# Kernel tuning notes

Measured on AMD Instinct MI355X. Metric: run time of the kernel, lower is better.

Reference implementation:

```python
import jax, jax.numpy as jnp
import numpy as np

B, N1, N2, E = 8, 32, 32, 256
H = 8                 # num_heads == args.vir_heads
KD = E // H           # key dim per head = 32
HD = E // H           # head dim (value_dim == embed_dim)
L = N1 * N2           # 1024 tokens
SCALING = KD ** -0.5
LN_EPS = 1e-5


def _rel_pos_2d():
    # RetNetRelPosDeform2D with zero offsets (vir_use_deformable=False)
    half = 1.0 / 10000.0 ** jnp.linspace(0.0, 1.0, KD // 2)
    angle = jnp.repeat(half, 2)                                   # (KD,) interleaved pairs
    decay = jnp.log(1.0 - 2.0 ** (-2.0 - 5.0 * jnp.arange(H, dtype=jnp.float32) / H))  # (H,)
    i1 = jnp.arange(N1, dtype=jnp.float32)
    i2 = jnp.arange(N2, dtype=jnp.float32)
    index_k = (i1[:, None] + i2[None, :]).reshape(L)              # (L,)
    sin_k = jnp.sin(index_k[:, None] * angle[None, :])            # (L, KD)
    cos_k = jnp.cos(index_k[:, None] * angle[None, :])
    # zero offsets => index_q == index_k, broadcast over (B, H)
    sin_q = sin_k[None, None]                                     # (1,1,L,KD)
    cos_q = cos_k[None, None]
    # Manhattan distance decay mask on the 2D grid
    d = (jnp.abs(i1[:, None, None, None] - i1[None, None, :, None])
         + jnp.abs(i2[None, :, None, None] - i2[None, None, None, :])).reshape(L, L)
    mask = jnp.exp(d[None, :, :] * decay[:, None, None])          # (H, L, L)
    mask = jnp.nan_to_num(mask)
    mask = mask / jnp.sqrt(mask.sum(-1, keepdims=True))
    return sin_q, cos_q, sin_k, cos_k, mask


def rotate_every_two(x):
    x1 = x[..., ::2]
    x2 = x[..., 1::2]
    return jnp.stack((-x2, x1), axis=-1).reshape(x.shape)


def theta_shift(x, sin, cos):
    return x * cos + rotate_every_two(x) * sin


def setup_inputs() -> dict:
    key = jax.random.key(0)
    ks = jax.random.split(key, 5)
    gain_qkv = 2.0 ** -2.5 * (6.0 / (E + E)) ** 0.5  # xavier_uniform bound scale
    gain_o = 2.0 ** -1 * (6.0 / (E + E)) ** 0.5
    x = jax.random.normal(ks[0], (B, N1, N2, E), dtype=jnp.float32)
    Wq = jax.random.uniform(ks[1], (E, E), jnp.float32, -gain_qkv, gain_qkv)
    Wk = jax.random.uniform(ks[2], (E, E), jnp.float32, -gain_qkv, gain_qkv)
    Wv = jax.random.uniform(ks[3], (E, E), jnp.float32, -gain_qkv, gain_qkv)
    Wo = jax.random.uniform(ks[4], (E, E), jnp.float32, -gain_o, gain_o)
    ln_g = jnp.ones((HD,), jnp.float32)
    ln_b = jnp.zeros((HD,), jnp.float32)
    return {"x": x, "Wq": Wq, "Wk": Wk, "Wv": Wv, "Wo": Wo, "ln_g": ln_g, "ln_b": ln_b}


def reference(x, Wq, Wk, Wv, Wo, ln_g, ln_b):
    sin_q, cos_q, sin_k, cos_k, mask = _rel_pos_2d()
    xf = x.reshape(B, L, E)
    q = (xf @ Wq.T).reshape(B, L, H, KD).transpose(0, 2, 1, 3)    # (B,H,L,KD)
    k = (xf @ Wk.T * SCALING).reshape(B, L, H, KD).transpose(0, 2, 1, 3)
    vr = (xf @ Wv.T).reshape(B, L, H, HD).transpose(0, 2, 1, 3)   # (B,H,L,HD)
    qr = theta_shift(q, sin_q, cos_q)
    kr = theta_shift(k, sin_k[None, None], cos_k[None, None])
    qk = jnp.einsum('bhqd,bhkd->bhqk', qr, kr) * mask[None]       # (B,H,L,L)
    den = jnp.clip(jax.lax.stop_gradient(jnp.abs(qk)).sum(-1, keepdims=True), 1.0, 5e4)
    qk = qk / den
    out = jnp.einsum('bhqk,bhkd->bhqd', qk, vr).transpose(0, 2, 1, 3)  # (B,L,H,HD)
    mu = out.mean(-1, keepdims=True)
    var = out.var(-1, keepdims=True)
    out = (out - mu) / jnp.sqrt(var + LN_EPS) * ln_g + ln_b       # per-head LayerNorm
    out = jax.nn.gelu(out.reshape(B, L, H * HD), approximate=False)
    out = out @ Wo.T
    return out.reshape(B, N1, N2, E)
```

## Files before the change

### kernel.cpp

```cpp
#include <hip/hip_runtime.h>
#include <math.h>

typedef unsigned short u16;
typedef unsigned int u32;
typedef __bf16 bf16x8 __attribute__((ext_vector_type(8)));
typedef float f32x4 __attribute__((ext_vector_type(4)));

#define LOG2E 1.44269504088896f
#define SCALING 0.17677669529663687f
#define LOG2_10000 13.287712379549449f

__device__ __forceinline__ float bf2f(u16 v) {
    u32 u = ((u32)v) << 16; float f; __builtin_memcpy(&f, &u, 4); return f;
}
__device__ __forceinline__ u16 f2bf(float f) {
    u32 u; __builtin_memcpy(&u, &f, 4);
    u = u + 0x7FFFu + ((u >> 16) & 1u);
    return (u16)(u >> 16);
}
__device__ __forceinline__ f32x4 mfma16(bf16x8 a, bf16x8 b, f32x4 c) {
    return __builtin_amdgcn_mfma_f32_16x16x32_bf16(a, b, c, 0, 0, 0);
}
__device__ __forceinline__ float decay_l2(int h) {
    return logf(1.0f - exp2f(-2.0f - 0.625f * (float)h)) * LOG2E;
}

__global__ __launch_bounds__(256) void mask_rsq_kernel(float* __restrict__ rsq) {
    int gw = (blockIdx.x * 256 + threadIdx.x) >> 6;
    int lane = threadIdx.x & 63;
    int h = gw >> 10, q = gw & 1023;
    float dec = decay_l2(h);
    int q1 = q >> 5, q2 = q & 31;
    float s = 0.0f;
    for (int k = lane; k < 1024; k += 64) {
        int k1 = k >> 5, k2 = k & 31;
        float d = (float)(abs(q1 - k1) + abs(q2 - k2));
        s += exp2f(dec * d);
    }
#pragma unroll
    for (int m = 32; m; m >>= 1) s += __shfl_xor(s, m);
    if (lane == 0) rsq[gw] = rsqrtf(s);
}

__global__ __launch_bounds__(256) void mask_build_kernel(const float* __restrict__ rsq,
                                                         u16* __restrict__ mask) {
    int t = blockIdx.x * 256 + threadIdx.x;
    int row = t >> 7;
    int k0 = (t & 127) << 3;
    int h = row >> 10, q = row & 1023;
    float dec = decay_l2(h);
    float r = rsq[row];
    int q1 = q >> 5, q2 = q & 31;
    int k1 = k0 >> 5, k2b = k0 & 31;
    union { int4 v; u16 s[8]; } tmp;
#pragma unroll
    for (int i = 0; i < 8; i++) {
        float d = (float)(abs(q1 - k1) + abs(q2 - (k2b + i)));
        tmp.s[i] = f2bf(exp2f(dec * d) * r);
    }
    *(int4*)&mask[(long)row * 1024 + k0] = tmp.v;
}

template<int AF32>
__global__ __launch_bounds__(256) void gemm_bt_kernel(
    const void* __restrict__ Av,
    const float* __restrict__ W0, const float* __restrict__ W1, const float* __restrict__ W2,
    u16* __restrict__ O0, u16* __restrict__ O1, u16* __restrict__ O2,
    float* __restrict__ Of, int mode_base) {
    __shared__ u16 As[64 * 136];
    __shared__ u16 Ws[64 * 136];
    int z = blockIdx.z;
    const float* W = (z == 0) ? W0 : (z == 1) ? W1 : W2;
    u16* O = (z == 0) ? O0 : (z == 1) ? O1 : O2;
    int mode = mode_base + z;
    int r0 = blockIdx.x * 64, n0 = blockIdx.y * 64;
    int tid = threadIdx.x;
    int w = tid >> 6, lane = tid & 63, ln = lane & 15, quad = lane >> 4;
    f32x4 acc[4] = {};
#pragma unroll
    for (int ch = 0; ch < 2; ch++) {
        int k0 = ch * 128;
        if (ch) __syncthreads();
#pragma unroll
        for (int i = 0; i < 8; i++) {
            int c = tid + i * 256;
            int row = c >> 5, seg = c & 31;
            float4 wv = *(const float4*)&W[(long)(n0 + row) * 256 + k0 + seg * 4];
            union { int2 v; u16 s[4]; } t;
            t.s[0] = f2bf(wv.x); t.s[1] = f2bf(wv.y); t.s[2] = f2bf(wv.z); t.s[3] = f2bf(wv.w);
            *(int2*)&Ws[row * 136 + seg * 4] = t.v;
        }
        if (AF32) {
            const float* A = (const float*)Av;
#pragma unroll
            for (int i = 0; i < 8; i++) {
                int c = tid + i * 256;
                int row = c >> 5, seg = c & 31;
                float4 av = *(const float4*)&A[(long)(r0 + row) * 256 + k0 + seg * 4];
                union { int2 v; u16 s[4]; } t;
                t.s[0] = f2bf(av.x); t.s[1] = f2bf(av.y); t.s[2] = f2bf(av.z); t.s[3] = f2bf(av.w);
                *(int2*)&As[row * 136 + seg * 4] = t.v;
            }
        } else {
            const u16* A = (const u16*)Av;
#pragma unroll
            for (int i = 0; i < 4; i++) {
                int c = tid + i * 256;
                int row = c >> 4, seg = c & 15;
                *(int4*)&As[row * 136 + seg * 8] = *(const int4*)&A[(long)(r0 + row) * 256 + k0 + seg * 8];
            }
        }
        __syncthreads();
#pragma unroll
        for (int kt = 0; kt < 4; kt++) {
            bf16x8 a = *(const bf16x8*)&As[(w * 16 + ln) * 136 + kt * 32 + quad * 8];
#pragma unroll
            for (int nt = 0; nt < 4; nt++) {
                bf16x8 b = *(const bf16x8*)&Ws[(nt * 16 + ln) * 136 + kt * 32 + quad * 8];
                acc[nt] = mfma16(a, b, acc[nt]);
            }
        }
    }
    int rowg = r0 + w * 16 + quad * 4;
    if (mode == 3) {
#pragma unroll
        for (int nt = 0; nt < 4; nt++) {
            int e = n0 + nt * 16 + ln;
#pragma unroll
            for (int r = 0; r < 4; r++)
                Of[(long)(rowg + r) * 256 + e] = acc[nt][r];
        }
        return;
    }
    float scl = (mode == 1) ? SCALING : 1.0f;
#pragma unroll
    for (int nt = 0; nt < 4; nt++) {
        int e = n0 + nt * 16 + ln;
        int d = e & 31, hh = e >> 5;
        float ang = exp2f(-LOG2_10000 * (1.0f / 15.0f) * (float)(d >> 1));
#pragma unroll
        for (int r = 0; r < 4; r++) {
            int gi = rowg + r;
            int b = gi >> 10, l = gi & 1023;
            float v = acc[nt][r] * scl;
            float p = __shfl_xor(v, 1);
            float res;
            if (mode == 2) {
                res = v;
            } else {
                float idx = (float)((l >> 5) + (l & 31));
                float sv, cv;
                __sincosf(idx * ang, &sv, &cv);
                res = (d & 1) ? (v * cv + p * sv) : (v * cv - p * sv);
            }
            O[(((long)(b * 8 + hh)) * 1024 + l) * 32 + d] = f2bf(res);
        }
    }
}

__global__ __launch_bounds__(256) void attn_kernel(
    const u16* __restrict__ qr, const u16* __restrict__ kr, const u16* __restrict__ vr,
    const u16* __restrict__ mask, const float* __restrict__ lng, const float* __restrict__ lnb,
    u16* __restrict__ out) {
    __shared__ u16 Qs[64 * 40];
    __shared__ u16 Ks[64 * 40];
    __shared__ u16 Vt[32 * 72];
    __shared__ u16 Ps[64 * 72];
    int b = blockIdx.z, h = blockIdx.y, q0 = blockIdx.x * 64;
    int tid = threadIdx.x, w = tid >> 6, lane = tid & 63, ln = lane & 15, quad = lane >> 4;
    long bh = b * 8 + h;
    const u16* qb = qr + bh * 32768;
    const u16* kb = kr + bh * 32768;
    const u16* vb = vr + bh * 32768;
    const u16* mb = mask + (long)h * 1048576;
    {
        int row = tid >> 2, seg = tid & 3;
        *(int4*)&Qs[row * 40 + seg * 8] = *(const int4*)&qb[(q0 + row) * 32 + seg * 8];
    }
    __syncthreads();
    int m0 = w * 16;
    bf16x8 aq = *(const bf16x8*)&Qs[(m0 + ln) * 40 + quad * 8];
    f32x4 accO[2] = {};
    float den[4] = {0.f, 0.f, 0.f, 0.f};
    for (int kt = 0; kt < 16; kt++) {
        int k0 = kt * 64;
        {
            int row = tid >> 2, seg = tid & 3;
            *(int4*)&Ks[row * 40 + seg * 8] = *(const int4*)&kb[(k0 + row) * 32 + seg * 8];
            union { int4 v; u16 s[8]; } vv;
            vv.v = *(const int4*)&vb[(k0 + row) * 32 + seg * 8];
#pragma unroll
            for (int i = 0; i < 8; i++) Vt[(seg * 8 + i) * 72 + row] = vv.s[i];
        }
        __syncthreads();
        f32x4 zero = {};
#pragma unroll
        for (int nt = 0; nt < 4; nt++) {
            bf16x8 bk = *(const bf16x8*)&Ks[(nt * 16 + ln) * 40 + quad * 8];
            f32x4 s = mfma16(aq, bk, zero);
            int col = nt * 16 + ln;
            const u16* mrow = mb + (long)(q0 + m0 + quad * 4) * 1024 + k0 + col;
#pragma unroll
            for (int r = 0; r < 4; r++) {
                float p = s[r] * bf2f(mrow[(long)r * 1024]);
                den[r] += fabsf(p);
                Ps[(m0 + quad * 4 + r) * 72 + col] = f2bf(p);
            }
        }
#pragma unroll
        for (int c2 = 0; c2 < 2; c2++) {
            bf16x8 ap = *(const bf16x8*)&Ps[(m0 + ln) * 72 + c2 * 32 + quad * 8];
#pragma unroll
            for (int nv = 0; nv < 2; nv++) {
                bf16x8 bv = *(const bf16x8*)&Vt[(nv * 16 + ln) * 72 + c2 * 32 + quad * 8];
                accO[nv] = mfma16(ap, bv, accO[nv]);
            }
        }
        __syncthreads();
    }
#pragma unroll
    for (int m = 1; m < 16; m <<= 1)
#pragma unroll
        for (int r = 0; r < 4; r++) den[r] += __shfl_xor(den[r], m);
    float o[2][4], s1[4], s2[4];
#pragma unroll
    for (int r = 0; r < 4; r++) {
        float id = 1.0f / fminf(fmaxf(den[r], 1.0f), 50000.0f);
        o[0][r] = accO[0][r] * id;
        o[1][r] = accO[1][r] * id;
        s1[r] = o[0][r] + o[1][r];
        s2[r] = o[0][r] * o[0][r] + o[1][r] * o[1][r];
    }
#pragma unroll
    for (int m = 1; m < 16; m <<= 1)
#pragma unroll
        for (int r = 0; r < 4; r++) {
            s1[r] += __shfl_xor(s1[r], m);
            s2[r] += __shfl_xor(s2[r], m);
        }
    float g[2] = {lng[ln], lng[16 + ln]};
    float bb[2] = {lnb[ln], lnb[16 + ln]};
#pragma unroll
    for (int r = 0; r < 4; r++) {
        float mean = s1[r] * (1.0f / 32.0f);
        float var = s2[r] * (1.0f / 32.0f) - mean * mean;
        float rstd = rsqrtf(var + 1e-5f);
        int l = q0 + m0 + quad * 4 + r;
#pragma unroll
        for (int nv = 0; nv < 2; nv++) {
            float x = (o[nv][r] - mean) * rstd * g[nv] + bb[nv];
            float ge = 0.5f * x * (1.0f + erff(x * 0.70710678118654752f));
            out[((long)(b * 1024 + l)) * 256 + h * 32 + nv * 16 + ln] = f2bf(ge);
        }
    }
}

extern "C" void kernel_launch(void* const* d_in, const int* in_sizes, int n_in,
                              void* d_out, int out_size, void* d_ws, size_t ws_size,
                              hipStream_t stream) {
    const float* x   = (const float*)d_in[0];
    const float* Wq  = (const float*)d_in[1];
    const float* Wk  = (const float*)d_in[2];
    const float* Wv  = (const float*)d_in[3];
    const float* Wo  = (const float*)d_in[4];
    const float* lng = (const float*)d_in[5];
    const float* lnb = (const float*)d_in[6];
    float* outp = (float*)d_out;

    u16* qr    = (u16*)d_ws;
    u16* kr    = qr + 2097152;
    u16* vr    = kr + 2097152;
    u16* attn  = vr + 2097152;
    u16* maskb = attn + 2097152;
    float* rsq = (float*)(maskb + 8388608);

    mask_rsq_kernel<<<2048, 256, 0, stream>>>(rsq);
    mask_build_kernel<<<4096, 256, 0, stream>>>(rsq, maskb);
    gemm_bt_kernel<1><<<dim3(128, 4, 3), 256, 0, stream>>>(x, Wq, Wk, Wv, qr, kr, vr, nullptr, 0);
    attn_kernel<<<dim3(16, 8, 8), 256, 0, stream>>>(qr, kr, vr, maskb, lng, lnb, attn);
    gemm_bt_kernel<0><<<dim3(128, 4, 1), 256, 0, stream>>>(attn, Wo, Wo, Wo, nullptr, nullptr, nullptr, outp, 3);
}
```

Measured before the change: 137.9 us.

## Compute decay mask on the fly in attention and pre-convert inputs to bf16

Removes the two kernels that built a 16 MB bf16 decay mask and instead computes mask values inside the attention kernel. It uses a per-block exp2 table indexed by Manhattan distance and a separable row-sum normalisation (the sum factors into Ss[q1]*Ss[q2]). Adds a conversion kernel that casts x and all weights to bf16 once, so the GEMMs load bf16 directly. The GEMM grid is reordered so that blocks sharing the same A rows run adjacently. The aim is to cut mask bandwidth and launches, at the cost of extra LDS lookups and integer work in the attention inner loop.

After: 128.9 us. -6.5%, faster.

```diff
diff --git a/kernel.cpp b/kernel.cpp
--- a/kernel.cpp
+++ b/kernel.cpp
@@ -6,13 +6,10 @@
 typedef __bf16 bf16x8 __attribute__((ext_vector_type(8)));
 typedef float f32x4 __attribute__((ext_vector_type(4)));
 
+#define SCALING 0.17677669529663687f
 #define LOG2E 1.44269504088896f
-#define SCALING 0.17677669529663687f
 #define LOG2_10000 13.287712379549449f
 
-__device__ __forceinline__ float bf2f(u16 v) {
-    u32 u = ((u32)v) << 16; float f; __builtin_memcpy(&f, &u, 4); return f;
-}
 __device__ __forceinline__ u16 f2bf(float f) {
     u32 u; __builtin_memcpy(&u, &f, 4);
     u = u + 0x7FFFu + ((u >> 16) & 1u);
@@ -25,55 +22,40 @@
     return logf(1.0f - exp2f(-2.0f - 0.625f * (float)h)) * LOG2E;
 }
 
-__global__ __launch_bounds__(256) void mask_rsq_kernel(float* __restrict__ rsq) {
-    int gw = (blockIdx.x * 256 + threadIdx.x) >> 6;
-    int lane = threadIdx.x & 63;
-    int h = gw >> 10, q = gw & 1023;
-    float dec = decay_l2(h);
-    int q1 = q >> 5, q2 = q & 31;
-    float s = 0.0f;
-    for (int k = lane; k < 1024; k += 64) {
-        int k1 = k >> 5, k2 = k & 31;
-        float d = (float)(abs(q1 - k1) + abs(q2 - k2));
-        s += exp2f(dec * d);
-    }
-#pragma unroll
-    for (int m = 32; m; m >>= 1) s += __shfl_xor(s, m);
-    if (lane == 0) rsq[gw] = rsqrtf(s);
-}
-
-__global__ __launch_bounds__(256) void mask_build_kernel(const float* __restrict__ rsq,
-                                                         u16* __restrict__ mask) {
-    int t = blockIdx.x * 256 + threadIdx.x;
-    int row = t >> 7;
-    int k0 = (t & 127) << 3;
-    int h = row >> 10, q = row & 1023;
-    float dec = decay_l2(h);
-    float r = rsq[row];
-    int q1 = q >> 5, q2 = q & 31;
-    int k1 = k0 >> 5, k2b = k0 & 31;
-    union { int4 v; u16 s[8]; } tmp;
-#pragma unroll
-    for (int i = 0; i < 8; i++) {
-        float d = (float)(abs(q1 - k1) + abs(q2 - (k2b + i)));
-        tmp.s[i] = f2bf(exp2f(dec * d) * r);
-    }
-    *(int4*)&mask[(long)row * 1024 + k0] = tmp.v;
-}
-
-template<int AF32>
+__global__ __launch_bounds__(256) void cvt_kernel(
+    const float* __restrict__ x,
+    const float* __restrict__ Wq, const float* __restrict__ Wk,
+    const float* __restrict__ Wv, const float* __restrict__ Wo,
+    u16* __restrict__ xb, u16* __restrict__ wb) {
+    int bid = blockIdx.x;
+    const float* src; u16* dst; int off;
+    if (bid < 1024) { src = x; dst = xb; off = bid * 2048; }
+    else {
+        int wsel = (bid - 1024) >> 5;
+        src = (wsel == 0) ? Wq : (wsel == 1) ? Wk : (wsel == 2) ? Wv : Wo;
+        dst = wb + wsel * 65536;
+        off = ((bid - 1024) & 31) * 2048;
+    }
+    int i = off + threadIdx.x * 8;
+    float4 a = *(const float4*)&src[i];
+    float4 b = *(const float4*)&src[i + 4];
+    union { int4 v; u16 s[8]; } t;
+    t.s[0] = f2bf(a.x); t.s[1] = f2bf(a.y); t.s[2] = f2bf(a.z); t.s[3] = f2bf(a.w);
+    t.s[4] = f2bf(b.x); t.s[5] = f2bf(b.y); t.s[6] = f2bf(b.z); t.s[7] = f2bf(b.w);
+    *(int4*)&dst[i] = t.v;
+}
+
 __global__ __launch_bounds__(256) void gemm_bt_kernel(
-    const void* __restrict__ Av,
-    const float* __restrict__ W0, const float* __restrict__ W1, const float* __restrict__ W2,
+    const u16* __restrict__ A, const u16* __restrict__ Wb,
     u16* __restrict__ O0, u16* __restrict__ O1, u16* __restrict__ O2,
     float* __restrict__ Of, int mode_base) {
     __shared__ u16 As[64 * 136];
     __shared__ u16 Ws[64 * 136];
     int z = blockIdx.z;
-    const float* W = (z == 0) ? W0 : (z == 1) ? W1 : W2;
+    const u16* W = Wb + z * 65536;
     u16* O = (z == 0) ? O0 : (z == 1) ? O1 : O2;
     int mode = mode_base + z;
-    int r0 = blockIdx.x * 64, n0 = blockIdx.y * 64;
+    int n0 = blockIdx.x * 64, r0 = blockIdx.y * 64;
     int tid = threadIdx.x;
     int w = tid >> 6, lane = tid & 63, ln = lane & 15, quad = lane >> 4;
     f32x4 acc[4] = {};
@@ -82,33 +64,11 @@
         int k0 = ch * 128;
         if (ch) __syncthreads();
 #pragma unroll
-        for (int i = 0; i < 8; i++) {
+        for (int i = 0; i < 4; i++) {
             int c = tid + i * 256;
-            int row = c >> 5, seg = c & 31;
-            float4 wv = *(const float4*)&W[(long)(n0 + row) * 256 + k0 + seg * 4];
-            union { int2 v; u16 s[4]; } t;
-            t.s[0] = f2bf(wv.x); t.s[1] = f2bf(wv.y); t.s[2] = f2bf(wv.z); t.s[3] = f2bf(wv.w);
-            *(int2*)&Ws[row * 136 + seg * 4] = t.v;
-        }
-        if (AF32) {
-            const float* A = (const float*)Av;
-#pragma unroll
-            for (int i = 0; i < 8; i++) {
-                int c = tid + i * 256;
-                int row = c >> 5, seg = c & 31;
-                float4 av = *(const float4*)&A[(long)(r0 + row) * 256 + k0 + seg * 4];
-                union { int2 v; u16 s[4]; } t;
-                t.s[0] = f2bf(av.x); t.s[1] = f2bf(av.y); t.s[2] = f2bf(av.z); t.s[3] = f2bf(av.w);
-                *(int2*)&As[row * 136 + seg * 4] = t.v;
-            }
-        } else {
-            const u16* A = (const u16*)Av;
-#pragma unroll
-            for (int i = 0; i < 4; i++) {
-                int c = tid + i * 256;
-                int row = c >> 4, seg = c & 15;
-                *(int4*)&As[row * 136 + seg * 8] = *(const int4*)&A[(long)(r0 + row) * 256 + k0 + seg * 8];
-            }
+            int row = c >> 4, seg = c & 15;
+            *(int4*)&As[row * 136 + seg * 8] = *(const int4*)&A[(long)(r0 + row) * 256 + k0 + seg * 8];
+            *(int4*)&Ws[row * 136 + seg * 8] = *(const int4*)&W[(long)(n0 + row) * 256 + k0 + seg * 8];
         }
         __syncthreads();
 #pragma unroll
@@ -160,26 +120,50 @@
 
 __global__ __launch_bounds__(256) void attn_kernel(
     const u16* __restrict__ qr, const u16* __restrict__ kr, const u16* __restrict__ vr,
-    const u16* __restrict__ mask, const float* __restrict__ lng, const float* __restrict__ lnb,
+    const float* __restrict__ lng, const float* __restrict__ lnb,
     u16* __restrict__ out) {
     __shared__ u16 Qs[64 * 40];
     __shared__ u16 Ks[64 * 40];
     __shared__ u16 Vt[32 * 72];
     __shared__ u16 Ps[64 * 72];
+    __shared__ float Tt[64];
+    __shared__ float Ss[32];
+    __shared__ float rq[64];
     int b = blockIdx.z, h = blockIdx.y, q0 = blockIdx.x * 64;
     int tid = threadIdx.x, w = tid >> 6, lane = tid & 63, ln = lane & 15, quad = lane >> 4;
     long bh = b * 8 + h;
     const u16* qb = qr + bh * 32768;
     const u16* kb = kr + bh * 32768;
     const u16* vb = vr + bh * 32768;
-    const u16* mb = mask + (long)h * 1048576;
+    float dec = decay_l2(h);
     {
         int row = tid >> 2, seg = tid & 3;
         *(int4*)&Qs[row * 40 + seg * 8] = *(const int4*)&qb[(q0 + row) * 32 + seg * 8];
+        if (tid < 63) Tt[tid] = exp2f(dec * (float)tid);
+    }
+    __syncthreads();
+    if (tid < 32) {
+        float s = 0.0f;
+#pragma unroll
+        for (int b2 = 0; b2 < 32; b2++) s += Tt[abs(tid - b2)];
+        Ss[tid] = s;
+    }
+    __syncthreads();
+    if (tid < 64) {
+        int q = q0 + tid;
+        rq[tid] = rsqrtf(Ss[q >> 5] * Ss[q & 31]);
     }
     __syncthreads();
     int m0 = w * 16;
     bf16x8 aq = *(const bf16x8*)&Qs[(m0 + ln) * 40 + quad * 8];
+    int q1r[4], q2r[4]; float rqv[4];
+#pragma unroll
+    for (int r = 0; r < 4; r++) {
+        int qrow = m0 + quad * 4 + r;
+        int q = q0 + qrow;
+        q1r[r] = q >> 5; q2r[r] = q & 31;
+        rqv[r] = rq[qrow];
+    }
     f32x4 accO[2] = {};
     float den[4] = {0.f, 0.f, 0.f, 0.f};
     for (int kt = 0; kt < 16; kt++) {
@@ -199,10 +183,12 @@
             bf16x8 bk = *(const bf16x8*)&Ks[(nt * 16 + ln) * 40 + quad * 8];
             f32x4 s = mfma16(aq, bk, zero);
             int col = nt * 16 + ln;
-            const u16* mrow = mb + (long)(q0 + m0 + quad * 4) * 1024 + k0 + col;
+            int k = k0 + col, k1 = k >> 5, k2 = k & 31;
 #pragma unroll
             for (int r = 0; r < 4; r++) {
-                float p = s[r] * bf2f(mrow[(long)r * 1024]);
+                int d = abs(q1r[r] - k1) + abs(q2r[r] - k2);
+                float m = Tt[d] * rqv[r];
+                float p = s[r] * m;
                 den[r] += fabsf(p);
                 Ps[(m0 + quad * 4 + r) * 72 + col] = f2bf(p);
             }
@@ -267,16 +253,15 @@
     const float* lnb = (const float*)d_in[6];
     float* outp = (float*)d_out;
 
-    u16* qr    = (u16*)d_ws;
-    u16* kr    = qr + 2097152;
-    u16* vr    = kr + 2097152;
-    u16* attn  = vr + 2097152;
-    u16* maskb = attn + 2097152;
-    float* rsq = (float*)(maskb + 8388608);
-
-    mask_rsq_kernel<<<2048, 256, 0, stream>>>(rsq);
-    mask_build_kernel<<<4096, 256, 0, stream>>>(rsq, maskb);
-    gemm_bt_kernel<1><<<dim3(128, 4, 3), 256, 0, stream>>>(x, Wq, Wk, Wv, qr, kr, vr, nullptr, 0);
-    attn_kernel<<<dim3(16, 8, 8), 256, 0, stream>>>(qr, kr, vr, maskb, lng, lnb, attn);
-    gemm_bt_kernel<0><<<dim3(128, 4, 1), 256, 0, stream>>>(attn, Wo, Wo, Wo, nullptr, nullptr, nullptr, outp, 3);
-}
+    u16* xb   = (u16*)d_ws;
+    u16* wb   = xb + 2097152;
+    u16* qr   = wb + 262144;
+    u16* kr   = qr + 2097152;
+    u16* vr   = kr + 2097152;
+    u16* attn = vr + 2097152;
+
+    cvt_kernel<<<1152, 256, 0, stream>>>(x, Wq, Wk, Wv, Wo, xb, wb);
+    gemm_bt_kernel<<<dim3(4, 128, 3), 256, 0, stream>>>(xb, wb, qr, kr, vr, nullptr, 0);
+    attn_kernel<<<dim3(16, 8, 8), 256, 0, stream>>>(qr, kr, vr, lng, lnb, attn);
+    gemm_bt_kernel<<<dim3(4, 128, 1), 256, 0, stream>>>(attn, wb + 3 * 65536, nullptr, nullptr, nullptr, outp, 3);
+}
```
